# Kernel tuning notes

Hardware: AMD Instinct MI355X
Metric: run time of the kernel (lower is better)

## Reference

```python
import jax, jax.numpy as jnp
import numpy as np

N = 50000
E = 800000
IN_DIM, HID_DIM, EMB_DIM = 128, 256, 128


def _sage_conv(x, src, dst, Wp, bp, Wl, bl, Wr):
    # PyG SAGEConv(project=True, aggr='max'):
    #   x_proj = relu(x @ Wp + bp)            # projection before message passing
    #   aggr   = scatter_max(x_proj[src] -> dst)  (empty segments -> 0)
    #   out    = aggr @ Wl + bl + x @ Wr      # lin_l(aggr) + lin_r(root)
    x_proj = jax.nn.relu(x @ Wp + bp)                      # [N, in]
    msg = x_proj[src]                                      # [E, in] gather
    aggr = jax.ops.segment_max(msg, dst, num_segments=N)   # [N, in] scatter-max
    aggr = jnp.where(jnp.isneginf(aggr), 0.0, aggr)        # empty neighborhoods -> 0
    return aggr @ Wl + bl + x @ Wr


def setup_inputs() -> dict:
    key = jax.random.key(0)
    ks = jax.random.split(key, 12)
    s = 0.05
    return {
        "x": jax.random.normal(ks[0], (N, IN_DIM), dtype=jnp.float32),
        "edge_index": jax.random.randint(ks[1], (2, E), 0, N, dtype=jnp.int64),
        # layer 1 params
        "Wp1": jax.random.normal(ks[2], (IN_DIM, IN_DIM), dtype=jnp.float32) * s,
        "bp1": jnp.zeros((IN_DIM,), dtype=jnp.float32),
        "Wl1": jax.random.normal(ks[3], (IN_DIM, HID_DIM), dtype=jnp.float32) * s,
        "bl1": jnp.zeros((HID_DIM,), dtype=jnp.float32),
        "Wr1": jax.random.normal(ks[4], (IN_DIM, HID_DIM), dtype=jnp.float32) * s,
        # layer 2 params
        "Wp2": jax.random.normal(ks[5], (HID_DIM, HID_DIM), dtype=jnp.float32) * s,
        "bp2": jnp.zeros((HID_DIM,), dtype=jnp.float32),
        "Wl2": jax.random.normal(ks[6], (HID_DIM, EMB_DIM), dtype=jnp.float32) * s,
        "bl2": jnp.zeros((EMB_DIM,), dtype=jnp.float32),
        "Wr2": jax.random.normal(ks[7], (HID_DIM, EMB_DIM), dtype=jnp.float32) * s,
    }


def reference(x, edge_index, Wp1, bp1, Wl1, bl1, Wr1, Wp2, bp2, Wl2, bl2, Wr2):
    src, dst = edge_index[0], edge_index[1]
    h = jax.nn.relu(_sage_conv(x, src, dst, Wp1, bp1, Wl1, bl1, Wr1))
    h = jax.nn.relu(_sage_conv(h, src, dst, Wp2, bp2, Wl2, bl2, Wr2))
    return h
```

## Files before the change

### kernel.cpp

```cpp
#include <hip/hip_runtime.h>


typedef __attribute__((ext_vector_type(8))) short short8;
typedef __attribute__((ext_vector_type(4))) float f32x4;

#define ADJ_CAP 64

__device__ __forceinline__ unsigned short f2bf(float f) {
    unsigned int u = __float_as_uint(f);
    u += 0x7fffu + ((u >> 16) & 1u);
    return (unsigned short)(u >> 16);
}

__device__ __forceinline__ unsigned int pkmax(unsigned int a, unsigned int b) {
    unsigned int r;
    asm("v_pk_max_u16 %0, %1, %2" : "=v"(r) : "v"(a), "v"(b));
    return r;
}

__device__ __forceinline__ short8 pack8(const float4 f0, const float4 f1) {
    union { unsigned short u[8]; short8 v; } r;
    r.u[0] = f2bf(f0.x); r.u[1] = f2bf(f0.y); r.u[2] = f2bf(f0.z); r.u[3] = f2bf(f0.w);
    r.u[4] = f2bf(f1.x); r.u[5] = f2bf(f1.y); r.u[6] = f2bf(f1.z); r.u[7] = f2bf(f1.w);
    return r.v;
}

__global__ __launch_bounds__(256) void pack_all_kernel(
    const float* __restrict__ Wp1, const float* __restrict__ Wl1,
    const float* __restrict__ Wr1, const float* __restrict__ Wp2,
    const float* __restrict__ Wl2, const float* __restrict__ Wr2,
    unsigned short* __restrict__ P0, unsigned short* __restrict__ P1,
    unsigned short* __restrict__ P2, unsigned short* __restrict__ P3,
    unsigned short* __restrict__ P4, unsigned short* __restrict__ P5)
{
    const int idx = blockIdx.x * 256 + threadIdx.x;
    const float* W; unsigned short* P; int Nc, local;
    if      (idx <  16384) { W = Wp1; P = P0; Nc = 128; local = idx; }
    else if (idx <  49152) { W = Wl1; P = P1; Nc = 256; local = idx - 16384; }
    else if (idx <  81920) { W = Wr1; P = P2; Nc = 256; local = idx - 49152; }
    else if (idx < 147456) { W = Wp2; P = P3; Nc = 256; local = idx - 81920; }
    else if (idx < 180224) { W = Wl2; P = P4; Nc = 128; local = idx - 147456; }
    else if (idx < 212992) { W = Wr2; P = P5; Nc = 128; local = idx - 180224; }
    else return;
    const int k = local / Nc, c = local % Nc;
    P[((size_t)(k >> 3) * Nc + c) * 8 + (k & 7)] = f2bf(W[local]);
}

__global__ __launch_bounds__(256) void build_adj_kernel(
    const int* __restrict__ src, const int* __restrict__ dst,
    int* __restrict__ deg, int* __restrict__ padj, int E)
{
    const int e = blockIdx.x * 256 + threadIdx.x;
    if (e < E) {
        const int d = dst[e];
        const int pos = atomicAdd(&deg[d], 1);
        if (pos < ADJ_CAP) padj[(size_t)d * ADJ_CAP + pos] = src[e];
    }
}

__global__ __launch_bounds__(256) void gemm_proj_f32(
    const float* __restrict__ A,
    const unsigned short* __restrict__ W,
    const float* __restrict__ bias,
    unsigned short* __restrict__ outp,
    int M)
{
    constexpr int K = 128, N = 128, BK = 32, LDK = BK + 8;
    __shared__ unsigned short As[64 * LDK];

    const int tid  = threadIdx.x;
    const int lane = tid & 63;
    const int wave = tid >> 6;
    const int fr   = lane & 15;
    const int g    = lane >> 4;
    const int bm   = blockIdx.x * 64;
    const int wr   = (wave >> 1) * 32;
    const int wc   = (wave & 1) * 64;

    const f32x4 zero = {0.f, 0.f, 0.f, 0.f};
    f32x4 acc[2][4];
#pragma unroll
    for (int m = 0; m < 2; ++m)
#pragma unroll
        for (int n = 0; n < 4; ++n) acc[m][n] = zero;

    for (int kt = 0; kt < K / BK; ++kt) {
        if (kt) __syncthreads();
        {
            const int r = tid >> 2, q = tid & 3;
            const int gm = min(bm + r, M - 1);
            const float4 f0 = *reinterpret_cast<const float4*>(A + (size_t)gm * K + kt * BK + q * 8);
            const float4 f1 = *reinterpret_cast<const float4*>(A + (size_t)gm * K + kt * BK + q * 8 + 4);
            *reinterpret_cast<short8*>(&As[r * LDK + q * 8]) = pack8(f0, f1);
        }
        __syncthreads();
        short8 af[2];
#pragma unroll
        for (int m = 0; m < 2; ++m)
            af[m] = *reinterpret_cast<const short8*>(&As[(wr + m * 16 + fr) * LDK + g * 8]);
#pragma unroll
        for (int n = 0; n < 4; ++n) {
            const short8 bf = *reinterpret_cast<const short8*>(
                W + ((size_t)(kt * 4 + g) * N + wc + n * 16 + fr) * 8);
#pragma unroll
            for (int m = 0; m < 2; ++m)
                acc[m][n] = __builtin_amdgcn_mfma_f32_16x16x32_bf16(af[m], bf, acc[m][n], 0, 0, 0);
        }
    }

    float bv[4];
#pragma unroll
    for (int n = 0; n < 4; ++n) bv[n] = bias[wc + n * 16 + fr];
#pragma unroll
    for (int m = 0; m < 2; ++m)
#pragma unroll
        for (int j = 0; j < 4; ++j) {
            const int row = bm + wr + m * 16 + g * 4 + j;
            if (row < M)
#pragma unroll
                for (int n = 0; n < 4; ++n)
                    outp[(size_t)row * N + wc + n * 16 + fr] =
                        f2bf(fmaxf(acc[m][n][j] + bv[n], 0.f));
        }
}

template<int D>
__global__ __launch_bounds__(256) void gather_max_bf16(
    const unsigned short* __restrict__ p, const int* __restrict__ padj,
    const int* __restrict__ deg, unsigned short* __restrict__ aggr, int n)
{
    const int node = (blockIdx.x * 256 + threadIdx.x) >> 6;
    const int lane = threadIdx.x & 63;
    if (node >= n) return;
    int d = deg[node];
    if (d > ADJ_CAP) d = ADJ_CAP;
    const int* __restrict__ a = padj + (size_t)node * ADJ_CAP;

    if (D == 128) {
        const int q  = lane >> 4;
        const int ll = lane & 15;
        uint4 acc = make_uint4(0u, 0u, 0u, 0u);
        for (int e = 0; e < d; e += 16) {
            const int i0 = min(e + q,      d - 1);
            const int i1 = min(e + 4 + q,  d - 1);
            const int i2 = min(e + 8 + q,  d - 1);
            const int i3 = min(e + 12 + q, d - 1);
            const int r0 = a[i0], r1 = a[i1], r2 = a[i2], r3 = a[i3];
            const uint4 v0 = *reinterpret_cast<const uint4*>(p + (size_t)r0 * 128 + ll * 8);
            const uint4 v1 = *reinterpret_cast<const uint4*>(p + (size_t)r1 * 128 + ll * 8);
            const uint4 v2 = *reinterpret_cast<const uint4*>(p + (size_t)r2 * 128 + ll * 8);
            const uint4 v3 = *reinterpret_cast<const uint4*>(p + (size_t)r3 * 128 + ll * 8);
            acc.x = pkmax(acc.x, pkmax(pkmax(v0.x, v1.x), pkmax(v2.x, v3.x)));
            acc.y = pkmax(acc.y, pkmax(pkmax(v0.y, v1.y), pkmax(v2.y, v3.y)));
            acc.z = pkmax(acc.z, pkmax(pkmax(v0.z, v1.z), pkmax(v2.z, v3.z)));
            acc.w = pkmax(acc.w, pkmax(pkmax(v0.w, v1.w), pkmax(v2.w, v3.w)));
        }
        acc.x = pkmax(acc.x, (unsigned int)__shfl_xor((int)acc.x, 16, 64));
        acc.y = pkmax(acc.y, (unsigned int)__shfl_xor((int)acc.y, 16, 64));
        acc.z = pkmax(acc.z, (unsigned int)__shfl_xor((int)acc.z, 16, 64));
        acc.w = pkmax(acc.w, (unsigned int)__shfl_xor((int)acc.w, 16, 64));
        acc.x = pkmax(acc.x, (unsigned int)__shfl_xor((int)acc.x, 32, 64));
        acc.y = pkmax(acc.y, (unsigned int)__shfl_xor((int)acc.y, 32, 64));
        acc.z = pkmax(acc.z, (unsigned int)__shfl_xor((int)acc.z, 32, 64));
        acc.w = pkmax(acc.w, (unsigned int)__shfl_xor((int)acc.w, 32, 64));
        if (lane < 16)
            *reinterpret_cast<uint4*>(aggr + (size_t)node * 128 + ll * 8) = acc;
    } else {
        const int h  = lane >> 5;
        const int ll = lane & 31;
        uint4 acc = make_uint4(0u, 0u, 0u, 0u);
        for (int e = 0; e < d; e += 16) {
            const int i0 = min(e + h,      d - 1);
            const int i1 = min(e + 2 + h,  d - 1);
            const int i2 = min(e + 4 + h,  d - 1);
            const int i3 = min(e + 6 + h,  d - 1);
            const int i4 = min(e + 8 + h,  d - 1);
            const int i5 = min(e + 10 + h, d - 1);
            const int i6 = min(e + 12 + h, d - 1);
            const int i7 = min(e + 14 + h, d - 1);
            const int r0 = a[i0], r1 = a[i1], r2 = a[i2], r3 = a[i3];
            const int r4 = a[i4], r5 = a[i5], r6 = a[i6], r7 = a[i7];
            const uint4 v0 = *reinterpret_cast<const uint4*>(p + (size_t)r0 * 256 + ll * 8);
            const uint4 v1 = *reinterpret_cast<const uint4*>(p + (size_t)r1 * 256 + ll * 8);
            const uint4 v2 = *reinterpret_cast<const uint4*>(p + (size_t)r2 * 256 + ll * 8);
            const uint4 v3 = *reinterpret_cast<const uint4*>(p + (size_t)r3 * 256 + ll * 8);
            const uint4 v4 = *reinterpret_cast<const uint4*>(p + (size_t)r4 * 256 + ll * 8);
            const uint4 v5 = *reinterpret_cast<const uint4*>(p + (size_t)r5 * 256 + ll * 8);
            const uint4 v6 = *reinterpret_cast<const uint4*>(p + (size_t)r6 * 256 + ll * 8);
            const uint4 v7 = *reinterpret_cast<const uint4*>(p + (size_t)r7 * 256 + ll * 8);
            acc.x = pkmax(acc.x, pkmax(pkmax(pkmax(v0.x, v1.x), pkmax(v2.x, v3.x)),
                                        pkmax(pkmax(v4.x, v5.x), pkmax(v6.x, v7.x))));
            acc.y = pkmax(acc.y, pkmax(pkmax(pkmax(v0.y, v1.y), pkmax(v2.y, v3.y)),
                                        pkmax(pkmax(v4.y, v5.y), pkmax(v6.y, v7.y))));
            acc.z = pkmax(acc.z, pkmax(pkmax(pkmax(v0.z, v1.z), pkmax(v2.z, v3.z)),
                                        pkmax(pkmax(v4.z, v5.z), pkmax(v6.z, v7.z))));
            acc.w = pkmax(acc.w, pkmax(pkmax(pkmax(v0.w, v1.w), pkmax(v2.w, v3.w)),
                                        pkmax(pkmax(v4.w, v5.w), pkmax(v6.w, v7.w))));
        }
        acc.x = pkmax(acc.x, (unsigned int)__shfl_xor((int)acc.x, 32, 64));
        acc.y = pkmax(acc.y, (unsigned int)__shfl_xor((int)acc.y, 32, 64));
        acc.z = pkmax(acc.z, (unsigned int)__shfl_xor((int)acc.z, 32, 64));
        acc.w = pkmax(acc.w, (unsigned int)__shfl_xor((int)acc.w, 32, 64));
        if (lane < 32)
            *reinterpret_cast<uint4*>(aggr + (size_t)node * 256 + ll * 8) = acc;
    }
}

__global__ __launch_bounds__(256) void tail1_kernel(
    const unsigned short* __restrict__ a1,
    const float* __restrict__ x,
    const unsigned short* __restrict__ Wl,
    const unsigned short* __restrict__ Wr,
    const float* __restrict__ bl,
    const unsigned short* __restrict__ Wp2,
    const float* __restrict__ bp2,
    unsigned short* __restrict__ h1,
    unsigned short* __restrict__ p2,
    int M)
{
    constexpr int LDK = 128 + 8;
    constexpr int LDH = 256 + 8;
    __shared__ unsigned short As[64 * LDK];
    __shared__ unsigned short Hs[64 * LDH];

    const int tid  = threadIdx.x;
    const int lane = tid & 63;
    const int wave = tid >> 6;
    const int fr   = lane & 15;
    const int g    = lane >> 4;
    const int bm   = blockIdx.x * 64;
    const int wc   = wave * 64;

    const f32x4 zero = {0.f, 0.f, 0.f, 0.f};
    f32x4 acc[4][4];
#pragma unroll
    for (int m = 0; m < 4; ++m)
#pragma unroll
        for (int n = 0; n < 4; ++n) acc[m][n] = zero;

#pragma unroll
    for (int c = 0; c < 4; ++c) {
        const int t = tid + c * 256;
        const int r = t >> 4, q = t & 15;
        const int gm = min(bm + r, M - 1);
        *reinterpret_cast<short8*>(&As[r * LDK + q * 8]) =
            *reinterpret_cast<const short8*>(a1 + (size_t)gm * 128 + q * 8);
    }
    __syncthreads();
#pragma unroll
    for (int kt = 0; kt < 4; ++kt) {
        short8 af[4];
#pragma unroll
        for (int m = 0; m < 4; ++m)
            af[m] = *reinterpret_cast<const short8*>(&As[(m * 16 + fr) * LDK + kt * 32 + g * 8]);
#pragma unroll
        for (int n = 0; n < 4; ++n) {
            const short8 bf = *reinterpret_cast<const short8*>(
                Wl + ((size_t)(kt * 4 + g) * 256 + wc + n * 16 + fr) * 8);
#pragma unroll
            for (int m = 0; m < 4; ++m)
                acc[m][n] = __builtin_amdgcn_mfma_f32_16x16x32_bf16(af[m], bf, acc[m][n], 0, 0, 0);
        }
    }
    __syncthreads();
#pragma unroll
    for (int c = 0; c < 4; ++c) {
        const int t = tid + c * 256;
        const int r = t >> 4, q = t & 15;
        const int gm = min(bm + r, M - 1);
        const float4 f0 = *reinterpret_cast<const float4*>(x + (size_t)gm * 128 + q * 8);
        const float4 f1 = *reinterpret_cast<const float4*>(x + (size_t)gm * 128 + q * 8 + 4);
        *reinterpret_cast<short8*>(&As[r * LDK + q * 8]) = pack8(f0, f1);
    }
    __syncthreads();
#pragma unroll
    for (int kt = 0; kt < 4; ++kt) {
        short8 af[4];
#pragma unroll
        for (int m = 0; m < 4; ++m)
            af[m] = *reinterpret_cast<const short8*>(&As[(m * 16 + fr) * LDK + kt * 32 + g * 8]);
#pragma unroll
        for (int n = 0; n < 4; ++n) {
            const short8 bf = *reinterpret_cast<const short8*>(
                Wr + ((size_t)(kt * 4 + g) * 256 + wc + n * 16 + fr) * 8);
#pragma unroll
            for (int m = 0; m < 4; ++m)
                acc[m][n] = __builtin_amdgcn_mfma_f32_16x16x32_bf16(af[m], bf, acc[m][n], 0, 0, 0);
        }
    }

    {
        float bv[4];
#pragma unroll
        for (int n = 0; n < 4; ++n) bv[n] = bl[wc + n * 16 + fr];
#pragma unroll
        for (int m = 0; m < 4; ++m)
#pragma unroll
            for (int j = 0; j < 4; ++j) {
                const int rl = m * 16 + g * 4 + j;
#pragma unroll
                for (int n = 0; n < 4; ++n) {
                    const unsigned short hb = f2bf(fmaxf(acc[m][n][j] + bv[n], 0.f));
                    Hs[rl * LDH + wc + n * 16 + fr] = hb;
                    if (bm + rl < M)
                        h1[(size_t)(bm + rl) * 256 + wc + n * 16 + fr] = hb;
                }
            }
    }
    __syncthreads();

#pragma unroll
    for (int m = 0; m < 4; ++m)
#pragma unroll
        for (int n = 0; n < 4; ++n) acc[m][n] = zero;
#pragma unroll
    for (int kt = 0; kt < 8; ++kt) {
        short8 af[4];
#pragma unroll
        for (int m = 0; m < 4; ++m)
            af[m] = *reinterpret_cast<const short8*>(&Hs[(m * 16 + fr) * LDH + kt * 32 + g * 8]);
#pragma unroll
        for (int n = 0; n < 4; ++n) {
            const short8 bf = *reinterpret_cast<const short8*>(
                Wp2 + ((size_t)(kt * 4 + g) * 256 + wc + n * 16 + fr) * 8);
#pragma unroll
            for (int m = 0; m < 4; ++m)
                acc[m][n] = __builtin_amdgcn_mfma_f32_16x16x32_bf16(af[m], bf, acc[m][n], 0, 0, 0);
        }
    }
    {
        float bv[4];
#pragma unroll
        for (int n = 0; n < 4; ++n) bv[n] = bp2[wc + n * 16 + fr];
#pragma unroll
        for (int m = 0; m < 4; ++m)
#pragma unroll
            for (int j = 0; j < 4; ++j) {
                const int row = bm + m * 16 + g * 4 + j;
                if (row < M)
#pragma unroll
                    for (int n = 0; n < 4; ++n)
                        p2[(size_t)row * 256 + wc + n * 16 + fr] =
                            f2bf(fmaxf(acc[m][n][j] + bv[n], 0.f));
            }
    }
}

__global__ __launch_bounds__(256) void tail2_kernel(
    const unsigned short* __restrict__ a2,
    const unsigned short* __restrict__ h1,
    const unsigned short* __restrict__ Wl,
    const unsigned short* __restrict__ Wr,
    const float* __restrict__ bl,
    float* __restrict__ out, int M)
{
    constexpr int LDK = 256 + 8;
    __shared__ unsigned short As[64 * LDK];

    const int tid  = threadIdx.x;
    const int lane = tid & 63;
    const int wave = tid >> 6;
    const int fr   = lane & 15;
    const int g    = lane >> 4;
    const int bm   = blockIdx.x * 64;
    const int wc   = wave * 32;

    const f32x4 zero = {0.f, 0.f, 0.f, 0.f};
    f32x4 acc[4][2];
#pragma unroll
    for (int m = 0; m < 4; ++m)
#pragma unroll
        for (int n = 0; n < 2; ++n) acc[m][n] = zero;

#pragma unroll
    for (int ph = 0; ph < 2; ++ph) {
        const unsigned short* __restrict__ P = ph ? h1 : a2;
        const unsigned short* __restrict__ W = ph ? Wr : Wl;
        if (ph) __syncthreads();
#pragma unroll
        for (int c = 0; c < 8; ++c) {
            const int t = tid + c * 256;
            const int r = t >> 5, q = t & 31;
            const int gm = min(bm + r, M - 1);
            *reinterpret_cast<short8*>(&As[r * LDK + q * 8]) =
                *reinterpret_cast<const short8*>(P + (size_t)gm * 256 + q * 8);
        }
        __syncthreads();
#pragma unroll
        for (int kt = 0; kt < 8; ++kt) {
            short8 af[4];
#pragma unroll
            for (int m = 0; m < 4; ++m)
                af[m] = *reinterpret_cast<const short8*>(&As[(m * 16 + fr) * LDK + kt * 32 + g * 8]);
#pragma unroll
            for (int n = 0; n < 2; ++n) {
                const short8 bf = *reinterpret_cast<const short8*>(
                    W + ((size_t)(kt * 4 + g) * 128 + wc + n * 16 + fr) * 8);
#pragma unroll
                for (int m = 0; m < 4; ++m)
                    acc[m][n] = __builtin_amdgcn_mfma_f32_16x16x32_bf16(af[m], bf, acc[m][n], 0, 0, 0);
            }
        }
    }

    float bv[2];
#pragma unroll
    for (int n = 0; n < 2; ++n) bv[n] = bl[wc + n * 16 + fr];
#pragma unroll
    for (int m = 0; m < 4; ++m)
#pragma unroll
        for (int j = 0; j < 4; ++j) {
            const int row = bm + m * 16 + g * 4 + j;
            if (row < M)
#pragma unroll
                for (int n = 0; n < 2; ++n)
                    out[(size_t)row * 128 + wc + n * 16 + fr] =
                        fmaxf(acc[m][n][j] + bv[n], 0.f);
        }
}

extern "C" void kernel_launch(void* const* d_in, const int* in_sizes, int n_in,
                              void* d_out, int out_size, void* d_ws, size_t ws_size,
                              hipStream_t stream)
{
    const float* x   = (const float*)d_in[0];
    const int*   ei  = (const int*)d_in[1];
    const float* Wp1 = (const float*)d_in[2];
    const float* bp1 = (const float*)d_in[3];
    const float* Wl1 = (const float*)d_in[4];
    const float* bl1 = (const float*)d_in[5];
    const float* Wr1 = (const float*)d_in[6];
    const float* Wp2 = (const float*)d_in[7];
    const float* bp2 = (const float*)d_in[8];
    const float* Wl2 = (const float*)d_in[9];
    const float* bl2 = (const float*)d_in[10];
    const float* Wr2 = (const float*)d_in[11];
    float* out = (float*)d_out;

    const int M = in_sizes[0] / 128;
    const int E = in_sizes[1] / 2;
    const int* src = ei;
    const int* dst = ei + E;

    unsigned short* ws  = (unsigned short*)d_ws;
    unsigned short* p1b = ws;
    unsigned short* a1b = p1b + (size_t)M * 128;
    unsigned short* h1b = a1b + (size_t)M * 128;
    unsigned short* p2b = h1b + (size_t)M * 256;
    unsigned short* a2b = p2b + (size_t)M * 256;
    unsigned short* wpk = a2b + (size_t)M * 256;
    unsigned short* Wp1p = wpk;
    unsigned short* Wl1p = Wp1p + 128 * 128;
    unsigned short* Wr1p = Wl1p + 128 * 256;
    unsigned short* Wp2p = Wr1p + 128 * 256;
    unsigned short* Wl2p = Wp2p + 256 * 256;
    unsigned short* Wr2p = Wl2p + 256 * 128;
    unsigned short* endu = Wr2p + 256 * 128;
    size_t int_off = ((size_t)(endu - ws) * 2 + 15) & ~(size_t)15;
    int* padj = (int*)((char*)d_ws + int_off);
    int* deg  = padj + (size_t)M * ADJ_CAP;

    const dim3 blk(256);
    const int eb = (E + 255) / 256;
    const int gb = (M + 3) / 4;
    const int mb64 = (M + 63) / 64;

    pack_all_kernel<<<(212992 + 255) / 256, blk, 0, stream>>>(
        Wp1, Wl1, Wr1, Wp2, Wl2, Wr2, Wp1p, Wl1p, Wr1p, Wp2p, Wl2p, Wr2p);
    hipMemsetAsync(deg, 0, (size_t)M * sizeof(int), stream);
    build_adj_kernel<<<eb, blk, 0, stream>>>(src, dst, deg, padj, E);

    gemm_proj_f32<<<mb64, blk, 0, stream>>>(x, Wp1p, bp1, p1b, M);
    gather_max_bf16<128><<<gb, blk, 0, stream>>>(p1b, padj, deg, a1b, M);
    tail1_kernel<<<mb64, blk, 0, stream>>>(
        a1b, x, Wl1p, Wr1p, bl1, Wp2p, bp2, h1b, p2b, M);

    gather_max_bf16<256><<<gb, blk, 0, stream>>>(p2b, padj, deg, a2b, M);
    tail2_kernel<<<mb64, blk, 0, stream>>>(
        a2b, h1b, Wl2p, Wr2p, bl2, out, M);
}
```

Baseline: 200.0 us.

## Merge adjacency build into projection GEMM launch and stage epilogue stores through LDS

The adjacency-building work is folded into the first projection GEMM as extra blocks of one launch, which removes a kernel launch and lets the two independent jobs run at the same time. The tail kernels now write their results into shared memory first and then store whole rows with wide vector writes. Before, each thread wrote scattered 2-byte or 4-byte elements to global memory. tail1 reuses one shared buffer for the inputs and hidden tiles, which lowers LDS use and may raise occupancy, at the cost of extra barriers.

```diff
diff --git a/kernel.cpp b/kernel.cpp
--- a/kernel.cpp
+++ b/kernel.cpp
@@ -46,25 +46,25 @@
     P[((size_t)(k >> 3) * Nc + c) * 8 + (k & 7)] = f2bf(W[local]);
 }
 
-__global__ __launch_bounds__(256) void build_adj_kernel(
-    const int* __restrict__ src, const int* __restrict__ dst,
-    int* __restrict__ deg, int* __restrict__ padj, int E)
-{
-    const int e = blockIdx.x * 256 + threadIdx.x;
-    if (e < E) {
-        const int d = dst[e];
-        const int pos = atomicAdd(&deg[d], 1);
-        if (pos < ADJ_CAP) padj[(size_t)d * ADJ_CAP + pos] = src[e];
-    }
-}
-
-__global__ __launch_bounds__(256) void gemm_proj_f32(
+__global__ __launch_bounds__(256) void adjproj_kernel(
     const float* __restrict__ A,
     const unsigned short* __restrict__ W,
     const float* __restrict__ bias,
     unsigned short* __restrict__ outp,
-    int M)
+    int M, int mbProj,
+    const int* __restrict__ src, const int* __restrict__ dst,
+    int* __restrict__ deg, int* __restrict__ padj, int E)
 {
+    if ((int)blockIdx.x >= mbProj) {
+        const int e = (blockIdx.x - mbProj) * 256 + threadIdx.x;
+        if (e < E) {
+            const int d = dst[e];
+            const int pos = atomicAdd(&deg[d], 1);
+            if (pos < ADJ_CAP) padj[(size_t)d * ADJ_CAP + pos] = src[e];
+        }
+        return;
+    }
+
     constexpr int K = 128, N = 128, BK = 32, LDK = BK + 8;
     __shared__ unsigned short As[64 * LDK];
 
@@ -218,9 +218,7 @@
     unsigned short* __restrict__ p2,
     int M)
 {
-    constexpr int LDK = 128 + 8;
-    constexpr int LDH = 256 + 8;
-    __shared__ unsigned short As[64 * LDK];
+    constexpr int LDH = 264;
     __shared__ unsigned short Hs[64 * LDH];
 
     const int tid  = threadIdx.x;
@@ -243,7 +241,7 @@
         const int t = tid + c * 256;
         const int r = t >> 4, q = t & 15;
         const int gm = min(bm + r, M - 1);
-        *reinterpret_cast<short8*>(&As[r * LDK + q * 8]) =
+        *reinterpret_cast<short8*>(&Hs[r * LDH + q * 8]) =
             *reinterpret_cast<const short8*>(a1 + (size_t)gm * 128 + q * 8);
     }
     __syncthreads();
@@ -252,7 +250,7 @@
         short8 af[4];
 #pragma unroll
         for (int m = 0; m < 4; ++m)
-            af[m] = *reinterpret_cast<const short8*>(&As[(m * 16 + fr) * LDK + kt * 32 + g * 8]);
+            af[m] = *reinterpret_cast<const short8*>(&Hs[(m * 16 + fr) * LDH + kt * 32 + g * 8]);
 #pragma unroll
         for (int n = 0; n < 4; ++n) {
             const short8 bf = *reinterpret_cast<const short8*>(
@@ -270,7 +268,7 @@
         const int gm = min(bm + r, M - 1);
         const float4 f0 = *reinterpret_cast<const float4*>(x + (size_t)gm * 128 + q * 8);
         const float4 f1 = *reinterpret_cast<const float4*>(x + (size_t)gm * 128 + q * 8 + 4);
-        *reinterpret_cast<short8*>(&As[r * LDK + q * 8]) = pack8(f0, f1);
+        *reinterpret_cast<short8*>(&Hs[r * LDH + q * 8]) = pack8(f0, f1);
     }
     __syncthreads();
 #pragma unroll
@@ -278,7 +276,7 @@
         short8 af[4];
 #pragma unroll
         for (int m = 0; m < 4; ++m)
-            af[m] = *reinterpret_cast<const short8*>(&As[(m * 16 + fr) * LDK + kt * 32 + g * 8]);
+            af[m] = *reinterpret_cast<const short8*>(&Hs[(m * 16 + fr) * LDH + kt * 32 + g * 8]);
 #pragma unroll
         for (int n = 0; n < 4; ++n) {
             const short8 bf = *reinterpret_cast<const short8*>(
@@ -288,6 +286,7 @@
                 acc[m][n] = __builtin_amdgcn_mfma_f32_16x16x32_bf16(af[m], bf, acc[m][n], 0, 0, 0);
         }
     }
+    __syncthreads();
 
     {
         float bv[4];
@@ -299,15 +298,21 @@
             for (int j = 0; j < 4; ++j) {
                 const int rl = m * 16 + g * 4 + j;
 #pragma unroll
-                for (int n = 0; n < 4; ++n) {
-                    const unsigned short hb = f2bf(fmaxf(acc[m][n][j] + bv[n], 0.f));
-                    Hs[rl * LDH + wc + n * 16 + fr] = hb;
-                    if (bm + rl < M)
-                        h1[(size_t)(bm + rl) * 256 + wc + n * 16 + fr] = hb;
-                }
+                for (int n = 0; n < 4; ++n)
+                    Hs[rl * LDH + wc + n * 16 + fr] =
+                        f2bf(fmaxf(acc[m][n][j] + bv[n], 0.f));
             }
     }
     __syncthreads();
+
+#pragma unroll
+    for (int c = 0; c < 8; ++c) {
+        const int id = tid + c * 256;
+        const int r = id >> 5, q = id & 31;
+        if (bm + r < M)
+            *reinterpret_cast<short8*>(h1 + (size_t)(bm + r) * 256 + q * 8) =
+                *reinterpret_cast<const short8*>(&Hs[r * LDH + q * 8]);
+    }
 
 #pragma unroll
     for (int m = 0; m < 4; ++m)
@@ -328,6 +333,8 @@
                 acc[m][n] = __builtin_amdgcn_mfma_f32_16x16x32_bf16(af[m], bf, acc[m][n], 0, 0, 0);
         }
     }
+    __syncthreads();
+
     {
         float bv[4];
 #pragma unroll
@@ -336,13 +343,21 @@
         for (int m = 0; m < 4; ++m)
 #pragma unroll
             for (int j = 0; j < 4; ++j) {
-                const int row = bm + m * 16 + g * 4 + j;
-                if (row < M)
-#pragma unroll
-                    for (int n = 0; n < 4; ++n)
-                        p2[(size_t)row * 256 + wc + n * 16 + fr] =
-                            f2bf(fmaxf(acc[m][n][j] + bv[n], 0.f));
+                const int rl = m * 16 + g * 4 + j;
+#pragma unroll
+                for (int n = 0; n < 4; ++n)
+                    Hs[rl * LDH + wc + n * 16 + fr] =
+                        f2bf(fmaxf(acc[m][n][j] + bv[n], 0.f));
             }
+    }
+    __syncthreads();
+#pragma unroll
+    for (int c = 0; c < 8; ++c) {
+        const int id = tid + c * 256;
+        const int r = id >> 5, q = id & 31;
+        if (bm + r < M)
+            *reinterpret_cast<short8*>(p2 + (size_t)(bm + r) * 256 + q * 8) =
+                *reinterpret_cast<const short8*>(&Hs[r * LDH + q * 8]);
     }
 }
 
@@ -354,8 +369,8 @@
     const float* __restrict__ bl,
     float* __restrict__ out, int M)
 {
-    constexpr int LDK = 256 + 8;
-    __shared__ unsigned short As[64 * LDK];
+    constexpr int LDH = 264;
+    __shared__ unsigned short As[64 * LDH];
 
     const int tid  = threadIdx.x;
     const int lane = tid & 63;
@@ -382,7 +397,7 @@
             const int t = tid + c * 256;
             const int r = t >> 5, q = t & 31;
             const int gm = min(bm + r, M - 1);
-            *reinterpret_cast<short8*>(&As[r * LDK + q * 8]) =
+            *reinterpret_cast<short8*>(&As[r * LDH + q * 8]) =
                 *reinterpret_cast<const short8*>(P + (size_t)gm * 256 + q * 8);
         }
         __syncthreads();
@@ -391,7 +406,7 @@
             short8 af[4];
 #pragma unroll
             for (int m = 0; m < 4; ++m)
-                af[m] = *reinterpret_cast<const short8*>(&As[(m * 16 + fr) * LDK + kt * 32 + g * 8]);
+                af[m] = *reinterpret_cast<const short8*>(&As[(m * 16 + fr) * LDH + kt * 32 + g * 8]);
 #pragma unroll
             for (int n = 0; n < 2; ++n) {
                 const short8 bf = *reinterpret_cast<const short8*>(
@@ -402,21 +417,32 @@
             }
         }
     }
-
-    float bv[2];
-#pragma unroll
-    for (int n = 0; n < 2; ++n) bv[n] = bl[wc + n * 16 + fr];
-#pragma unroll
-    for (int m = 0; m < 4; ++m)
-#pragma unroll
-        for (int j = 0; j < 4; ++j) {
-            const int row = bm + m * 16 + g * 4 + j;
-            if (row < M)
+    __syncthreads();
+
+    float* Fs = reinterpret_cast<float*>(As);
+    {
+        float bv[2];
+#pragma unroll
+        for (int n = 0; n < 2; ++n) bv[n] = bl[wc + n * 16 + fr];
+#pragma unroll
+        for (int m = 0; m < 4; ++m)
+#pragma unroll
+            for (int j = 0; j < 4; ++j) {
+                const int rl = m * 16 + g * 4 + j;
 #pragma unroll
                 for (int n = 0; n < 2; ++n)
-                    out[(size_t)row * 128 + wc + n * 16 + fr] =
-                        fmaxf(acc[m][n][j] + bv[n], 0.f);
-        }
+                    Fs[rl * 132 + wc + n * 16 + fr] = fmaxf(acc[m][n][j] + bv[n], 0.f);
+            }
+    }
+    __syncthreads();
+#pragma unroll
+    for (int c = 0; c < 8; ++c) {
+        const int id = tid + c * 256;
+        const int r = id >> 5, q = id & 31;
+        if (bm + r < M)
+            *reinterpret_cast<float4*>(out + (size_t)(bm + r) * 128 + q * 4) =
+                *reinterpret_cast<const float4*>(&Fs[r * 132 + q * 4]);
+    }
 }
 
 extern "C" void kernel_launch(void* const* d_in, const int* in_sizes, int n_in,
@@ -468,9 +494,9 @@
     pack_all_kernel<<<(212992 + 255) / 256, blk, 0, stream>>>(
         Wp1, Wl1, Wr1, Wp2, Wl2, Wr2, Wp1p, Wl1p, Wr1p, Wp2p, Wl2p, Wr2p);
     hipMemsetAsync(deg, 0, (size_t)M * sizeof(int), stream);
-    build_adj_kernel<<<eb, blk, 0, stream>>>(src, dst, deg, padj, E);
-
-    gemm_proj_f32<<<mb64, blk, 0, stream>>>(x, Wp1p, bp1, p1b, M);
+    adjproj_kernel<<<mb64 + eb, blk, 0, stream>>>(
+        x, Wp1p, bp1, p1b, M, mb64, src, dst, deg, padj, E);
+
     gather_max_bf16<128><<<gb, blk, 0, stream>>>(p1b, padj, deg, a1b, M);
     tail1_kernel<<<mb64, blk, 0, stream>>>(
         a1b, x, Wl1p, Wr1p, bl1, Wp2p, bp2, h1b, p2b, M);
```

New measurement: 222.4 us. 1.11x slower.

## Store projected features column-sliced and gather per slice for cache locality

Applied to the files above, without the earlier changes.

The projection GEMM and tail1 now write their bf16 outputs in a column-sliced layout (8 slices of 16 or 32 columns). The max-aggregation kernel launches one block per (node group, slice) and gathers only a narrow slice per neighbor, with one edge per lane group and a shuffle reduction. The goal is to shrink the randomly accessed working set so neighbor reads hit cache. In exchange, adjacency lists are read once per slice and each gather touches only 32–64 bytes. Because slice is the fastest-varying block index, slices run concurrently, which may defeat the locality goal.

```diff
diff --git a/kernel.cpp b/kernel.cpp
--- a/kernel.cpp
+++ b/kernel.cpp
@@ -15,6 +15,21 @@
 __device__ __forceinline__ unsigned int pkmax(unsigned int a, unsigned int b) {
     unsigned int r;
     asm("v_pk_max_u16 %0, %1, %2" : "=v"(r) : "v"(a), "v"(b));
+    return r;
+}
+
+__device__ __forceinline__ uint4 pkmax4(uint4 a, const uint4 b) {
+    a.x = pkmax(a.x, b.x); a.y = pkmax(a.y, b.y);
+    a.z = pkmax(a.z, b.z); a.w = pkmax(a.w, b.w);
+    return a;
+}
+
+__device__ __forceinline__ uint4 shflx4(const uint4 a, int m) {
+    uint4 r;
+    r.x = (unsigned int)__shfl_xor((int)a.x, m, 64);
+    r.y = (unsigned int)__shfl_xor((int)a.y, m, 64);
+    r.z = (unsigned int)__shfl_xor((int)a.z, m, 64);
+    r.w = (unsigned int)__shfl_xor((int)a.w, m, 64);
     return r;
 }
 
@@ -118,91 +133,60 @@
             const int row = bm + wr + m * 16 + g * 4 + j;
             if (row < M)
 #pragma unroll
-                for (int n = 0; n < 4; ++n)
-                    outp[(size_t)row * N + wc + n * 16 + fr] =
+                for (int n = 0; n < 4; ++n) {
+                    const int slice = (wc + n * 16) >> 4;
+                    outp[(size_t)slice * M * 16 + (size_t)row * 16 + fr] =
                         f2bf(fmaxf(acc[m][n][j] + bv[n], 0.f));
+                }
         }
 }
 
 template<int D>
-__global__ __launch_bounds__(256) void gather_max_bf16(
+__global__ __launch_bounds__(256) void gather_sliced(
     const unsigned short* __restrict__ p, const int* __restrict__ padj,
-    const int* __restrict__ deg, unsigned short* __restrict__ aggr, int n)
-{
-    const int node = (blockIdx.x * 256 + threadIdx.x) >> 6;
-    const int lane = threadIdx.x & 63;
+    const int* __restrict__ deg, unsigned short* __restrict__ aggr,
+    int n, size_t sstride)
+{
+    const int slice = blockIdx.x & 7;
+    const int node  = (blockIdx.x >> 3) * 4 + (threadIdx.x >> 6);
+    const int lane  = threadIdx.x & 63;
     if (node >= n) return;
     int d = deg[node];
     if (d > ADJ_CAP) d = ADJ_CAP;
     const int* __restrict__ a = padj + (size_t)node * ADJ_CAP;
+    const unsigned short* __restrict__ sb = p + (size_t)slice * sstride;
 
     if (D == 128) {
-        const int q  = lane >> 4;
-        const int ll = lane & 15;
+        const int e = lane >> 1, q = lane & 1;
         uint4 acc = make_uint4(0u, 0u, 0u, 0u);
-        for (int e = 0; e < d; e += 16) {
-            const int i0 = min(e + q,      d - 1);
-            const int i1 = min(e + 4 + q,  d - 1);
-            const int i2 = min(e + 8 + q,  d - 1);
-            const int i3 = min(e + 12 + q, d - 1);
-            const int r0 = a[i0], r1 = a[i1], r2 = a[i2], r3 = a[i3];
-            const uint4 v0 = *reinterpret_cast<const uint4*>(p + (size_t)r0 * 128 + ll * 8);
-            const uint4 v1 = *reinterpret_cast<const uint4*>(p + (size_t)r1 * 128 + ll * 8);
-            const uint4 v2 = *reinterpret_cast<const uint4*>(p + (size_t)r2 * 128 + ll * 8);
-            const uint4 v3 = *reinterpret_cast<const uint4*>(p + (size_t)r3 * 128 + ll * 8);
-            acc.x = pkmax(acc.x, pkmax(pkmax(v0.x, v1.x), pkmax(v2.x, v3.x)));
-            acc.y = pkmax(acc.y, pkmax(pkmax(v0.y, v1.y), pkmax(v2.y, v3.y)));
-            acc.z = pkmax(acc.z, pkmax(pkmax(v0.z, v1.z), pkmax(v2.z, v3.z)));
-            acc.w = pkmax(acc.w, pkmax(pkmax(v0.w, v1.w), pkmax(v2.w, v3.w)));
-        }
-        acc.x = pkmax(acc.x, (unsigned int)__shfl_xor((int)acc.x, 16, 64));
-        acc.y = pkmax(acc.y, (unsigned int)__shfl_xor((int)acc.y, 16, 64));
-        acc.z = pkmax(acc.z, (unsigned int)__shfl_xor((int)acc.z, 16, 64));
-        acc.w = pkmax(acc.w, (unsigned int)__shfl_xor((int)acc.w, 16, 64));
-        acc.x = pkmax(acc.x, (unsigned int)__shfl_xor((int)acc.x, 32, 64));
-        acc.y = pkmax(acc.y, (unsigned int)__shfl_xor((int)acc.y, 32, 64));
-        acc.z = pkmax(acc.z, (unsigned int)__shfl_xor((int)acc.z, 32, 64));
-        acc.w = pkmax(acc.w, (unsigned int)__shfl_xor((int)acc.w, 32, 64));
-        if (lane < 16)
-            *reinterpret_cast<uint4*>(aggr + (size_t)node * 128 + ll * 8) = acc;
+        for (int e0 = 0; e0 < d; e0 += 32) {
+            const int idx = min(e0 + e, d - 1);
+            const int s = __builtin_nontemporal_load(a + idx);
+            const uint4 v = *reinterpret_cast<const uint4*>(sb + (size_t)s * 16 + q * 8);
+            acc = pkmax4(acc, v);
+        }
+        acc = pkmax4(acc, shflx4(acc, 2));
+        acc = pkmax4(acc, shflx4(acc, 4));
+        acc = pkmax4(acc, shflx4(acc, 8));
+        acc = pkmax4(acc, shflx4(acc, 16));
+        acc = pkmax4(acc, shflx4(acc, 32));
+        if (lane < 2)
+            *reinterpret_cast<uint4*>(aggr + (size_t)node * 128 + slice * 16 + q * 8) = acc;
     } else {
-        const int h  = lane >> 5;
-        const int ll = lane & 31;
+        const int e = lane >> 2, q = lane & 3;
         uint4 acc = make_uint4(0u, 0u, 0u, 0u);
-        for (int e = 0; e < d; e += 16) {
-            const int i0 = min(e + h,      d - 1);
-            const int i1 = min(e + 2 + h,  d - 1);
-            const int i2 = min(e + 4 + h,  d - 1);
-            const int i3 = min(e + 6 + h,  d - 1);
-            const int i4 = min(e + 8 + h,  d - 1);
-            const int i5 = min(e + 10 + h, d - 1);
-            const int i6 = min(e + 12 + h, d - 1);
-            const int i7 = min(e + 14 + h, d - 1);
-            const int r0 = a[i0], r1 = a[i1], r2 = a[i2], r3 = a[i3];
-            const int r4 = a[i4], r5 = a[i5], r6 = a[i6], r7 = a[i7];
-            const uint4 v0 = *reinterpret_cast<const uint4*>(p + (size_t)r0 * 256 + ll * 8);
-            const uint4 v1 = *reinterpret_cast<const uint4*>(p + (size_t)r1 * 256 + ll * 8);
-            const uint4 v2 = *reinterpret_cast<const uint4*>(p + (size_t)r2 * 256 + ll * 8);
-            const uint4 v3 = *reinterpret_cast<const uint4*>(p + (size_t)r3 * 256 + ll * 8);
-            const uint4 v4 = *reinterpret_cast<const uint4*>(p + (size_t)r4 * 256 + ll * 8);
-            const uint4 v5 = *reinterpret_cast<const uint4*>(p + (size_t)r5 * 256 + ll * 8);
-            const uint4 v6 = *reinterpret_cast<const uint4*>(p + (size_t)r6 * 256 + ll * 8);
-            const uint4 v7 = *reinterpret_cast<const uint4*>(p + (size_t)r7 * 256 + ll * 8);
-            acc.x = pkmax(acc.x, pkmax(pkmax(pkmax(v0.x, v1.x), pkmax(v2.x, v3.x)),
-                                        pkmax(pkmax(v4.x, v5.x), pkmax(v6.x, v7.x))));
-            acc.y = pkmax(acc.y, pkmax(pkmax(pkmax(v0.y, v1.y), pkmax(v2.y, v3.y)),
-                                        pkmax(pkmax(v4.y, v5.y), pkmax(v6.y, v7.y))));
-            acc.z = pkmax(acc.z, pkmax(pkmax(pkmax(v0.z, v1.z), pkmax(v2.z, v3.z)),
-                                        pkmax(pkmax(v4.z, v5.z), pkmax(v6.z, v7.z))));
-            acc.w = pkmax(acc.w, pkmax(pkmax(pkmax(v0.w, v1.w), pkmax(v2.w, v3.w)),
-                                        pkmax(pkmax(v4.w, v5.w), pkmax(v6.w, v7.w))));
-        }
-        acc.x = pkmax(acc.x, (unsigned int)__shfl_xor((int)acc.x, 32, 64));
-        acc.y = pkmax(acc.y, (unsigned int)__shfl_xor((int)acc.y, 32, 64));
-        acc.z = pkmax(acc.z, (unsigned int)__shfl_xor((int)acc.z, 32, 64));
-        acc.w = pkmax(acc.w, (unsigned int)__shfl_xor((int)acc.w, 32, 64));
-        if (lane < 32)
-            *reinterpret_cast<uint4*>(aggr + (size_t)node * 256 + ll * 8) = acc;
+        for (int e0 = 0; e0 < d; e0 += 16) {
+            const int idx = min(e0 + e, d - 1);
+            const int s = __builtin_nontemporal_load(a + idx);
+            const uint4 v = *reinterpret_cast<const uint4*>(sb + (size_t)s * 32 + q * 8);
+            acc = pkmax4(acc, v);
+        }
+        acc = pkmax4(acc, shflx4(acc, 4));
+        acc = pkmax4(acc, shflx4(acc, 8));
+        acc = pkmax4(acc, shflx4(acc, 16));
+        acc = pkmax4(acc, shflx4(acc, 32));
+        if (lane < 4)
+            *reinterpret_cast<uint4*>(aggr + (size_t)node * 256 + slice * 32 + q * 8) = acc;
     }
 }
 
@@ -339,9 +323,13 @@
                 const int row = bm + m * 16 + g * 4 + j;
                 if (row < M)
 #pragma unroll
-                    for (int n = 0; n < 4; ++n)
-                        p2[(size_t)row * 256 + wc + n * 16 + fr] =
+                    for (int n = 0; n < 4; ++n) {
+                        const int col    = wc + n * 16;
+                        const int slice  = col >> 5;
+                        const int within = (col & 31) + fr;
+                        p2[(size_t)slice * M * 32 + (size_t)row * 32 + within] =
                             f2bf(fmaxf(acc[m][n][j] + bv[n], 0.f));
+                    }
             }
     }
 }
@@ -462,7 +450,7 @@
 
     const dim3 blk(256);
     const int eb = (E + 255) / 256;
-    const int gb = (M + 3) / 4;
+    const int gbs = 8 * ((M + 3) / 4);
     const int mb64 = (M + 63) / 64;
 
     pack_all_kernel<<<(212992 + 255) / 256, blk, 0, stream>>>(
@@ -471,11 +459,13 @@
     build_adj_kernel<<<eb, blk, 0, stream>>>(src, dst, deg, padj, E);
 
     gemm_proj_f32<<<mb64, blk, 0, stream>>>(x, Wp1p, bp1, p1b, M);
-    gather_max_bf16<128><<<gb, blk, 0, stream>>>(p1b, padj, deg, a1b, M);
+    gather_sliced<128><<<gbs, blk, 0, stream>>>(
+        p1b, padj, deg, a1b, M, (size_t)M * 16);
     tail1_kernel<<<mb64, blk, 0, stream>>>(
         a1b, x, Wl1p, Wr1p, bl1, Wp2p, bp2, h1b, p2b, M);
 
-    gather_max_bf16<256><<<gb, blk, 0, stream>>>(p2b, padj, deg, a2b, M);
+    gather_sliced<256><<<gbs, blk, 0, stream>>>(
+        p2b, padj, deg, a2b, M, (size_t)M * 32);
     tail2_kernel<<<mb64, blk, 0, stream>>>(
         a2b, h1b, Wl2p, Wr2p, bl2, out, M);
 }
```

Measured after the change: 351.0 us. +75.5%, slower.
